# Kernel tuning notes

Measured on AMD Instinct MI355X. Metric: run time of the kernel, lower is better.

The kernel has to match this reference:

```python
import jax, jax.numpy as jnp
import numpy as np

N = 50000          # nodes
H = 202            # hidden = text(200) + selector(2)
E = 100000         # edges per forward edge type
FWD_TYPES = 3      # forward edge types; backward doubles to 6
LAYER_TIMESTEPS = (2,)
POS_MAX = 1024


def _pos_table():
    # transformer-style sinusoidal embeddings for positions [0, POS_MAX)
    inv_freq = 1.0 / (10000.0 ** (jnp.arange(0, H, 2, dtype=jnp.float32) / H))  # [H/2]
    pos = jnp.arange(POS_MAX, dtype=jnp.float32)
    sinusoid = pos[:, None] * inv_freq[None, :]                                  # [POS_MAX, H/2]
    return jnp.concatenate([jnp.sin(sinusoid), jnp.cos(sinusoid)], axis=-1)      # [POS_MAX, H]


def setup_inputs() -> dict:
    key = jax.random.key(0)
    ks = jax.random.split(key, 11)
    L = len(LAYER_TIMESTEPS)
    s = 0.1
    return {
        "node_states": jax.random.normal(ks[0], (N, H), jnp.float32),
        "edge_lists": jax.random.randint(ks[1], (FWD_TYPES, E, 2), 0, N, jnp.int32),
        "pos_lists": jax.random.randint(ks[2], (FWD_TYPES, E), 0, POS_MAX, jnp.int32),
        "msg_W": jax.random.normal(ks[3], (L, H, 2 * FWD_TYPES * H), jnp.float32) * s,
        "msg_b": jax.random.normal(ks[4], (L, 2 * FWD_TYPES * H), jnp.float32) * s,
        "pos_W": jax.random.normal(ks[5], (L, H, H), jnp.float32) * s,
        "pos_b": jax.random.normal(ks[6], (L, H), jnp.float32) * s,
        "gru_Wih": jax.random.normal(ks[7], (L, 3 * H, H), jnp.float32) * s,
        "gru_Whh": jax.random.normal(ks[8], (L, 3 * H, H), jnp.float32) * s,
        "gru_bih": jax.random.normal(ks[9], (L, 3 * H), jnp.float32) * s,
        "gru_bhh": jax.random.normal(ks[10], (L, 3 * H), jnp.float32) * s,
    }


def _ggnn(node_states, src, tgt, pos, divisor,
          msg_W, msg_b, pos_W, pos_b, gru_Wih, gru_Whh, gru_bih, gru_bhh):
    ET = src.shape[0]  # 2 * FWD_TYPES edge types (forward + backward)
    h = node_states
    pos_table = _pos_table()
    for l, steps in enumerate(LAYER_TIMESTEPS):
        # 2*sigmoid(pos_transform(position_embs)) gating, per position id
        gate = 2.0 * jax.nn.sigmoid(pos_table @ pos_W[l] + pos_b[l])  # [POS_MAX, H]
        for _ in range(steps):
            # fused per-edge-type transforms: [N, ET*H] chunked -> [N, ET, H]
            prop = (h @ msg_W[l] + msg_b[l]).reshape(h.shape[0], ET, H)
            messages = jnp.zeros_like(h)
            for i in range(ET):  # small fixed loop over edge types
                m = prop[:, i, :][src[i]] * gate[pos[i]]  # [E, H]
                messages = messages.at[tgt[i]].add(m)
            messages = messages / divisor  # mean aggregation
            # nn.GRUCell(messages, h)
            gi = messages @ gru_Wih[l].T + gru_bih[l]
            gh = h @ gru_Whh[l].T + gru_bhh[l]
            ir, iz, inn = jnp.split(gi, 3, axis=1)
            hr, hz, hn = jnp.split(gh, 3, axis=1)
            r = jax.nn.sigmoid(ir + hr)
            z = jax.nn.sigmoid(iz + hz)
            n = jnp.tanh(inn + r * hn)
            h = (1.0 - z) * n + z * h
    return h


def reference(node_states, edge_lists, pos_lists, msg_W, msg_b, pos_W, pos_b,
              gru_Wih, gru_Whh, gru_bih, gru_bhh):
    # backward edges = flipped forward edges; pos lists duplicated
    src = jnp.concatenate([edge_lists[:, :, 0], edge_lists[:, :, 1]], axis=0)  # [6, E]
    tgt = jnp.concatenate([edge_lists[:, :, 1], edge_lists[:, :, 0]], axis=0)  # [6, E]
    pos = jnp.clip(jnp.concatenate([pos_lists, pos_lists], axis=0), 0, POS_MAX - 1)
    # target bincount over all edge types; zero counts -> 1
    counts = jnp.zeros((node_states.shape[0],), jnp.float32).at[tgt.reshape(-1)].add(1.0)
    divisor = jnp.where(counts == 0, 1.0, counts)[:, None]
    out = _ggnn(node_states, src, tgt, pos, divisor, msg_W, msg_b, pos_W, pos_b,
                gru_Wih, gru_Whh, gru_bih, gru_bhh)
    return out, node_states
```

## Files before the change

### kernel.cpp

```cpp
#include <hip/hip_runtime.h>

#define NN 50000
#define HH 202
#define EE 100000
#define PMX 1024
#define NKT 7
#define PKS2 (16 * NKT * 64 * 8)
#define NEDG (6 * EE)
#define AFR (4 * NKT * 64 * 8)

typedef __attribute__((ext_vector_type(8))) short short8;
typedef __attribute__((ext_vector_type(4))) float v4f;

__device__ __forceinline__ float sigf(float x) { return 1.0f / (1.0f + expf(-x)); }

__device__ __forceinline__ unsigned short f2bf(float x) {
    unsigned int u = __float_as_uint(x);
    unsigned int r = (u + 0x7fffu + ((u >> 16) & 1u)) >> 16;
    return (unsigned short)r;
}
__device__ __forceinline__ float bf2f(unsigned short u) {
    return __uint_as_float(((unsigned int)u) << 16);
}

__device__ __forceinline__ int frag_off(int row, int k) {
    return (((row >> 4) * NKT + (k >> 5)) * 64 + ((k >> 3) & 3) * 16 + (row & 15)) * 8 + (k & 7);
}

__global__ void gate_kernel(const float* __restrict__ pos_W, const float* __restrict__ pos_b,
                            unsigned short* __restrict__ gate) {
    int p = blockIdx.x;
    __shared__ float pt[HH];
    int t = threadIdx.x;
    if (t < HH) {
        float v;
        if (t < 101) {
            float invf = expf(-(2.0f * t / 202.0f) * 9.210340371976184f);
            v = sinf((float)p * invf);
        } else {
            int k = t - 101;
            float invf = expf(-(2.0f * k / 202.0f) * 9.210340371976184f);
            v = cosf((float)p * invf);
        }
        pt[t] = v;
    }
    __syncthreads();
    for (int j = t; j < HH; j += blockDim.x) {
        float acc = pos_b[j];
        for (int k = 0; k < HH; ++k) acc += pt[k] * pos_W[k * HH + j];
        gate[p * HH + j] = f2bf(2.0f * sigf(acc));
    }
}

__global__ void pack_kernel(const float* __restrict__ S, int ldb, int row0, int col0, int mode,
                            unsigned short* __restrict__ BP) {
    int idx = blockIdx.x * blockDim.x + threadIdx.x;
    if (idx >= PKS2) return;
    int jj = idx & 7;
    int l = (idx >> 3) & 63;
    int r2 = idx >> 9;
    int cf = r2 / NKT, kt = r2 - cf * NKT;
    int k = kt * 32 + ((l >> 4) << 3) + jj;
    int j = cf * 16 + (l & 15);
    float v = 0.0f;
    if (k < HH && j < HH)
        v = mode ? S[(size_t)(row0 + j) * HH + k] : S[(size_t)k * ldb + col0 + j];
    BP[idx] = f2bf(v);
}

__global__ void count_kernel(const int* __restrict__ el, int* __restrict__ cnt) {
    int idx = blockIdx.x * blockDim.x + threadIdx.x;
    if (idx >= NEDG) return;
    int ty = idx / EE, e = idx - ty * EE;
    int2 pr = (ty < 3) ? reinterpret_cast<const int2*>(el)[ty * EE + e]
                       : reinterpret_cast<const int2*>(el)[(ty - 3) * EE + e];
    int tg = (ty < 3) ? pr.y : pr.x;
    atomicAdd(&cnt[tg], 1);
}

__global__ void scan1_kernel(const int* __restrict__ cnt, int* __restrict__ off,
                             int* __restrict__ bsum) {
    __shared__ int sd[256];
    int t = threadIdx.x, i = blockIdx.x * 256 + t;
    int v = (i < NN) ? cnt[i] : 0;
    sd[t] = v;
    __syncthreads();
    for (int s = 1; s < 256; s <<= 1) {
        int u = (t >= s) ? sd[t - s] : 0;
        __syncthreads();
        sd[t] += u;
        __syncthreads();
    }
    if (i < NN) off[i] = sd[t] - v;
    if (t == 255) bsum[blockIdx.x] = sd[255];
}

__global__ void scan2_kernel(int* __restrict__ bsum, int nb) {
    __shared__ int sd[256];
    int t = threadIdx.x;
    int v = (t < nb) ? bsum[t] : 0;
    sd[t] = v;
    __syncthreads();
    for (int s = 1; s < 256; s <<= 1) {
        int u = (t >= s) ? sd[t - s] : 0;
        __syncthreads();
        sd[t] += u;
        __syncthreads();
    }
    if (t < nb) bsum[t] = sd[t] - v;
}

__global__ void scan3_kernel(int* __restrict__ off, const int* __restrict__ bsum,
                             int* __restrict__ cursor) {
    int i = blockIdx.x * 256 + threadIdx.x;
    if (i < NN) {
        int o = off[i] + bsum[blockIdx.x];
        off[i] = o;
        cursor[i] = o;
    }
    if (i == 0) off[NN] = NEDG;
}

__global__ void inv_kernel(const int* __restrict__ cnt, float* __restrict__ inv) {
    int n = blockIdx.x * blockDim.x + threadIdx.x;
    if (n < NN) inv[n] = 1.0f / (float)max(cnt[n], 1);
}

__global__ void fill_kernel(const int* __restrict__ el, const int* __restrict__ pl,
                            int* __restrict__ cursor, int* __restrict__ edg) {
    int idx = blockIdx.x * blockDim.x + threadIdx.x;
    if (idx >= NEDG) return;
    int ty = idx / EE, e = idx - ty * EE;
    int s, tg;
    if (ty < 3) {
        int2 pr = reinterpret_cast<const int2*>(el)[ty * EE + e];
        s = pr.x; tg = pr.y;
    } else {
        int2 pr = reinterpret_cast<const int2*>(el)[(ty - 3) * EE + e];
        s = pr.y; tg = pr.x;
    }
    int p = pl[(ty % 3) * EE + e];
    p = min(max(p, 0), PMX - 1);
    int slot = atomicAdd(&cursor[tg], 1);
    edg[slot] = (s << 13) | (ty << 10) | p;
}

__global__ __launch_bounds__(512, 4) void gemm9(
    const void* __restrict__ Asrc, int a_is_f32,
    const unsigned short* __restrict__ BPbase, int npack,
    const float* __restrict__ bias,
    unsigned short* __restrict__ O0, unsigned short* __restrict__ O1, int split) {
    __shared__ alignas(16) unsigned short a_lds[AFR];
    __shared__ alignas(16) unsigned short c_lds[64 * HH];
    const int t = threadIdx.x;
    const int w = t >> 6;
    const int l = t & 63;
    const int lm = l & 15, lh = l >> 4;
    const int rowg = w >> 2, colg = w & 3;
    const int cs = colg * 4;
    const int base = blockIdx.x * 64;
    const int vrows = min(64, NN - base);
    const int nu4 = (vrows * 101) >> 2;

    if (a_is_f32) {
        const float* A = (const float*)Asrc;
        for (int idx = t; idx < 64 * 101; idx += 512) {
            int row = idx / 101;
            int c = idx - row * 101;
            int gn = base + row;
            float2 v = make_float2(0.f, 0.f);
            if (gn < NN) v = *reinterpret_cast<const float2*>(&A[(size_t)gn * HH + c * 2]);
            ushort2 bv; bv.x = f2bf(v.x); bv.y = f2bf(v.y);
            *reinterpret_cast<ushort2*>(&a_lds[frag_off(row, c * 2)]) = bv;
        }
    } else {
        const unsigned short* A = (const unsigned short*)Asrc;
        for (int idx = t; idx < 64 * 101; idx += 512) {
            int row = idx / 101;
            int c = idx - row * 101;
            int gn = base + row;
            ushort2 v; v.x = 0; v.y = 0;
            if (gn < NN) v = *reinterpret_cast<const ushort2*>(&A[(size_t)gn * HH + c * 2]);
            *reinterpret_cast<ushort2*>(&a_lds[frag_off(row, c * 2)]) = v;
        }
    }
    for (int idx = t; idx < 64 * 11; idx += 512) {
        int row = idx / 11;
        int c = idx - row * 11;
        ushort2 z; z.x = 0; z.y = 0;
        *reinterpret_cast<ushort2*>(&a_lds[frag_off(row, HH + c * 2)]) = z;
    }
    __syncthreads();

    const int aoff0 = (rowg * 2) * (NKT * 512) + l * 8;
    const int aoff1 = aoff0 + NKT * 512;

#pragma unroll 1
    for (int p = 0; p < npack; ++p) {
        const unsigned short* BP = BPbase + (size_t)p * PKS2 + (size_t)l * 8;
        v4f acc[4][2];
#pragma unroll
        for (int ci = 0; ci < 4; ++ci) {
            acc[ci][0] = (v4f){0.f, 0.f, 0.f, 0.f};
            acc[ci][1] = (v4f){0.f, 0.f, 0.f, 0.f};
        }

        short8 ac0 = *reinterpret_cast<const short8*>(&a_lds[aoff0]);
        short8 ac1 = *reinterpret_cast<const short8*>(&a_lds[aoff1]);
        short8 bc0 = *reinterpret_cast<const short8*>(BP + (size_t)(cs + 0) * NKT * 512);
        short8 bc1 = *reinterpret_cast<const short8*>(BP + (size_t)(cs + 1) * NKT * 512);
        short8 bc2 = *reinterpret_cast<const short8*>(BP + (size_t)(cs + 2) * NKT * 512);
        short8 bc3 = *reinterpret_cast<const short8*>(BP + (size_t)(cs + 3) * NKT * 512);

#pragma unroll
        for (int kt = 0; kt < NKT; ++kt) {
            const int kn = (kt + 1 < NKT) ? (kt + 1) : kt;
            const int ka = kn * 512;
            short8 an0 = *reinterpret_cast<const short8*>(&a_lds[aoff0 + ka]);
            short8 an1 = *reinterpret_cast<const short8*>(&a_lds[aoff1 + ka]);
            short8 bn0 = *reinterpret_cast<const short8*>(BP + (size_t)(cs + 0) * NKT * 512 + ka);
            short8 bn1 = *reinterpret_cast<const short8*>(BP + (size_t)(cs + 1) * NKT * 512 + ka);
            short8 bn2 = *reinterpret_cast<const short8*>(BP + (size_t)(cs + 2) * NKT * 512 + ka);
            short8 bn3 = *reinterpret_cast<const short8*>(BP + (size_t)(cs + 3) * NKT * 512 + ka);

            acc[0][0] = __builtin_amdgcn_mfma_f32_16x16x32_bf16(ac0, bc0, acc[0][0], 0, 0, 0);
            acc[0][1] = __builtin_amdgcn_mfma_f32_16x16x32_bf16(ac1, bc0, acc[0][1], 0, 0, 0);
            acc[1][0] = __builtin_amdgcn_mfma_f32_16x16x32_bf16(ac0, bc1, acc[1][0], 0, 0, 0);
            acc[1][1] = __builtin_amdgcn_mfma_f32_16x16x32_bf16(ac1, bc1, acc[1][1], 0, 0, 0);
            acc[2][0] = __builtin_amdgcn_mfma_f32_16x16x32_bf16(ac0, bc2, acc[2][0], 0, 0, 0);
            acc[2][1] = __builtin_amdgcn_mfma_f32_16x16x32_bf16(ac1, bc2, acc[2][1], 0, 0, 0);
            acc[3][0] = __builtin_amdgcn_mfma_f32_16x16x32_bf16(ac0, bc3, acc[3][0], 0, 0, 0);
            acc[3][1] = __builtin_amdgcn_mfma_f32_16x16x32_bf16(ac1, bc3, acc[3][1], 0, 0, 0);

            ac0 = an0; ac1 = an1;
            bc0 = bn0; bc1 = bn1; bc2 = bn2; bc3 = bn3;
        }

        __syncthreads();
#pragma unroll
        for (int ci = 0; ci < 4; ++ci) {
            int col = (cs + ci) * 16 + lm;
            if (col < HH) {
                float bb = bias ? bias[p * HH + col] : 0.0f;
#pragma unroll
                for (int rfi = 0; rfi < 2; ++rfi) {
#pragma unroll
                    for (int r = 0; r < 4; ++r)
                        c_lds[(rowg * 32 + rfi * 16 + lh * 4 + r) * HH + col] =
                            f2bf(acc[ci][rfi][r] + bb);
                }
            }
        }
        __syncthreads();

        unsigned short* slab = (p < split) ? O0 + (size_t)p * NN * HH
                                           : O1 + (size_t)(p - split) * NN * HH;
        uint4* dst = reinterpret_cast<uint4*>(slab + (size_t)base * HH);
        const uint4* srcp = reinterpret_cast<const uint4*>(c_lds);
        for (int i = t; i < nu4; i += 512) dst[i] = srcp[i];
    }
}

__global__ void agg_kernel(const unsigned short* __restrict__ CH0,
                           const unsigned short* __restrict__ CH45,
                           const int* __restrict__ off, const int* __restrict__ edg,
                           const unsigned short* __restrict__ gate,
                           const float* __restrict__ inv, unsigned short* __restrict__ msgb) {
    int n = blockIdx.x * 4 + (threadIdx.x >> 6);
    if (n >= NN) return;
    int lane = threadIdx.x & 63;
    int s0 = off[n], s1 = off[n + 1];
    int j0 = lane, j1 = lane + 64, j2 = lane + 128, j3 = lane + 192;
    bool j3ok = j3 < HH;
    float a0 = 0.f, a1 = 0.f, a2 = 0.f, a3 = 0.f;
    float b0 = 0.f, b1 = 0.f, b2 = 0.f, b3 = 0.f;
    int i = s0;
    for (; i + 1 < s1; i += 2) {
        int recA = edg[i], recB = edg[i + 1];
        int sA = recA >> 13, tyA = (recA >> 10) & 7, pA = recA & 1023;
        int sB = recB >> 13, tyB = (recB >> 10) & 7, pB = recB & 1023;
        const unsigned short* crA =
            ((tyA < 4) ? CH0 + (size_t)tyA * NN * HH : CH45 + (size_t)(tyA - 4) * NN * HH)
            + (size_t)sA * HH;
        const unsigned short* crB =
            ((tyB < 4) ? CH0 + (size_t)tyB * NN * HH : CH45 + (size_t)(tyB - 4) * NN * HH)
            + (size_t)sB * HH;
        const unsigned short* grA = gate + (size_t)pA * HH;
        const unsigned short* grB = gate + (size_t)pB * HH;
        a0 += bf2f(crA[j0]) * bf2f(grA[j0]);
        b0 += bf2f(crB[j0]) * bf2f(grB[j0]);
        a1 += bf2f(crA[j1]) * bf2f(grA[j1]);
        b1 += bf2f(crB[j1]) * bf2f(grB[j1]);
        a2 += bf2f(crA[j2]) * bf2f(grA[j2]);
        b2 += bf2f(crB[j2]) * bf2f(grB[j2]);
        if (j3ok) { a3 += bf2f(crA[j3]) * bf2f(grA[j3]);
                    b3 += bf2f(crB[j3]) * bf2f(grB[j3]); }
    }
    if (i < s1) {
        int rec = edg[i];
        int src = rec >> 13, ty = (rec >> 10) & 7, p = rec & 1023;
        const unsigned short* cr =
            ((ty < 4) ? CH0 + (size_t)ty * NN * HH : CH45 + (size_t)(ty - 4) * NN * HH)
            + (size_t)src * HH;
        const unsigned short* gr = gate + (size_t)p * HH;
        a0 += bf2f(cr[j0]) * bf2f(gr[j0]);
        a1 += bf2f(cr[j1]) * bf2f(gr[j1]);
        a2 += bf2f(cr[j2]) * bf2f(gr[j2]);
        if (j3ok) a3 += bf2f(cr[j3]) * bf2f(gr[j3]);
    }
    float iv = inv[n];
    unsigned short* mr = msgb + (size_t)n * HH;
    mr[j0] = f2bf((a0 + b0) * iv); mr[j1] = f2bf((a1 + b1) * iv);
    mr[j2] = f2bf((a2 + b2) * iv);
    if (j3ok) mr[j3] = f2bf((a3 + b3) * iv);
}

__global__ void gru_ew(float* __restrict__ h, const float* __restrict__ hsrc,
                       const unsigned short* __restrict__ GH,
                       const unsigned short* __restrict__ GIr,
                       const unsigned short* __restrict__ GIzn,
                       const float* __restrict__ bih, const float* __restrict__ bhh) {
    int n = blockIdx.x * 4 + (threadIdx.x >> 6);
    if (n >= NN) return;
    int lane = threadIdx.x & 63;
    const size_t NH = (size_t)NN * HH;
    const size_t ro = (size_t)n * HH;
    for (int j = lane; j < HH; j += 64) {
        float ghr = bf2f(GH[ro + j]);
        float ghz = bf2f(GH[NH + ro + j]);
        float ghn = bf2f(GH[2 * NH + ro + j]);
        float gir = bf2f(GIr[ro + j]);
        float giz = bf2f(GIzn[ro + j]);
        float gin = bf2f(GIzn[NH + ro + j]);
        float r = sigf(gir + ghr + bih[j] + bhh[j]);
        float z = sigf(giz + ghz + bih[202 + j] + bhh[202 + j]);
        float nn = tanhf(gin + bih[404 + j] + r * (ghn + bhh[404 + j]));
        h[ro + j] = (1.0f - z) * nn + z * hsrc[ro + j];
    }
}

extern "C" void kernel_launch(void* const* d_in, const int* in_sizes, int n_in,
                              void* d_out, int out_size, void* d_ws, size_t ws_size,
                              hipStream_t stream) {
    const float* node_states = (const float*)d_in[0];
    const int*   el          = (const int*)d_in[1];
    const int*   pl          = (const int*)d_in[2];
    const float* msg_W       = (const float*)d_in[3];
    const float* msg_b       = (const float*)d_in[4];
    const float* pos_W       = (const float*)d_in[5];
    const float* pos_b       = (const float*)d_in[6];
    const float* gWih        = (const float*)d_in[7];
    const float* gWhh        = (const float*)d_in[8];
    const float* gbih        = (const float*)d_in[9];
    const float* gbhh        = (const float*)d_in[10];

    float* out  = (float*)d_out;
    float* h    = out;
    float* out2 = out + (size_t)NN * HH;

    unsigned short* CH0  = (unsigned short*)d_ws;
    unsigned short* CH45 = (unsigned short*)out2;
    unsigned short* MSGB = CH0 + (size_t)4 * NN * HH;
    unsigned short* GATE = MSGB + (size_t)NN * HH;
    float* INV  = (float*)(GATE + (size_t)PMX * HH + 8);
    int* CNT    = (int*)(INV + NN);
    int* OFF    = CNT + NN;
    int* CUR    = OFF + NN + 4;
    int* BS     = CUR + NN;
    int* EDG    = BS + 256;
    unsigned short* BPA = (unsigned short*)(EDG + NEDG);
    unsigned short* BPp  = BPA;
    unsigned short* BPih = BPA + (size_t)6 * PKS2;
    unsigned short* BPhh = BPA + (size_t)9 * PKS2;

    const size_t NH = (size_t)NN * HH;
    hipMemsetAsync(CNT, 0, NN * sizeof(int), stream);
    gate_kernel<<<PMX, 256, 0, stream>>>(pos_W, pos_b, GATE);
    const int pkb = (PKS2 + 255) / 256;
    for (int ty = 0; ty < 6; ++ty)
        pack_kernel<<<pkb, 256, 0, stream>>>(msg_W, 1212, 0, ty * HH, 0, BPp + (size_t)ty * PKS2);
    pack_kernel<<<pkb, 256, 0, stream>>>(gWih, 0, 0,   0, 1, BPih);
    pack_kernel<<<pkb, 256, 0, stream>>>(gWih, 0, 202, 0, 1, BPih + PKS2);
    pack_kernel<<<pkb, 256, 0, stream>>>(gWih, 0, 404, 0, 1, BPih + 2 * PKS2);
    pack_kernel<<<pkb, 256, 0, stream>>>(gWhh, 0, 0,   0, 1, BPhh);
    pack_kernel<<<pkb, 256, 0, stream>>>(gWhh, 0, 202, 0, 1, BPhh + PKS2);
    pack_kernel<<<pkb, 256, 0, stream>>>(gWhh, 0, 404, 0, 1, BPhh + 2 * PKS2);

    const int nsb = (NN + 255) / 256;
    count_kernel<<<(NEDG + 255) / 256, 256, 0, stream>>>(el, CNT);
    scan1_kernel<<<nsb, 256, 0, stream>>>(CNT, OFF, BS);
    scan2_kernel<<<1, 256, 0, stream>>>(BS, nsb);
    scan3_kernel<<<nsb, 256, 0, stream>>>(OFF, BS, CUR);
    inv_kernel<<<nsb, 256, 0, stream>>>(CNT, INV);
    fill_kernel<<<(NEDG + 255) / 256, 256, 0, stream>>>(el, pl, CUR, EDG);

    const int gblocks = (NN + 63) / 64;
    const int ewblocks = (NN + 3) / 4;
    for (int step = 0; step < 2; ++step) {
        const float* hsrc = (step == 0) ? node_states : h;
        gemm9<<<gblocks, 512, 0, stream>>>(hsrc, 1, BPp, 6, msg_b, CH0, CH45, 4);
        agg_kernel<<<ewblocks, 256, 0, stream>>>(CH0, CH45, OFF, EDG, GATE, INV, MSGB);
        gemm9<<<gblocks, 512, 0, stream>>>(hsrc, 1, BPhh, 3, nullptr, CH0, nullptr, 4);
        gemm9<<<gblocks, 512, 0, stream>>>(MSGB, 0, BPih, 3, nullptr,
                                           CH0 + 3 * NH, CH45, 1);
        gru_ew<<<ewblocks, 256, 0, stream>>>(h, hsrc, CH0, CH0 + 3 * NH, CH45, gbih, gbhh);
    }
    hipMemcpyAsync(out2, node_states, NH * sizeof(float), hipMemcpyDeviceToDevice, stream);
}
```

Before: 660.1 us.

## Hold A tile in registers and compute 64x64 tiles per wave in GEMM

```diff
diff --git a/kernel.cpp b/kernel.cpp
--- a/kernel.cpp
+++ b/kernel.cpp
@@ -7,10 +7,11 @@
 #define NKT 7
 #define PKS2 (16 * NKT * 64 * 8)
 #define NEDG (6 * EE)
-#define AFR (4 * NKT * 64 * 8)
 
 typedef __attribute__((ext_vector_type(8))) short short8;
 typedef __attribute__((ext_vector_type(4))) float v4f;
+
+union U8 { unsigned int u[4]; short8 s; };
 
 __device__ __forceinline__ float sigf(float x) { return 1.0f / (1.0f + expf(-x)); }
 
@@ -23,8 +24,10 @@
     return __uint_as_float(((unsigned int)u) << 16);
 }
 
-__device__ __forceinline__ int frag_off(int row, int k) {
-    return (((row >> 4) * NKT + (k >> 5)) * 64 + ((k >> 3) & 3) * 16 + (row & 15)) * 8 + (k & 7);
+__device__ __forceinline__ unsigned int cvtpk(float lo, float hi) {
+    unsigned int r;
+    asm("v_cvt_pk_bf16_f32 %0, %1, %2" : "=v"(r) : "v"(lo), "v"(hi));
+    return r;
 }
 
 __global__ void gate_kernel(const float* __restrict__ pos_W, const float* __restrict__ pos_b,
@@ -145,68 +148,83 @@
     edg[slot] = (s << 13) | (ty << 10) | p;
 }
 
-__global__ __launch_bounds__(512, 4) void gemm9(
+__global__ __launch_bounds__(256, 2) void gemmR(
     const void* __restrict__ Asrc, int a_is_f32,
     const unsigned short* __restrict__ BPbase, int npack,
     const float* __restrict__ bias,
     unsigned short* __restrict__ O0, unsigned short* __restrict__ O1, int split) {
-    __shared__ alignas(16) unsigned short a_lds[AFR];
     __shared__ alignas(16) unsigned short c_lds[64 * HH];
     const int t = threadIdx.x;
     const int w = t >> 6;
     const int l = t & 63;
     const int lm = l & 15, lh = l >> 4;
-    const int rowg = w >> 2, colg = w & 3;
-    const int cs = colg * 4;
+    const int cs = w * 4;
     const int base = blockIdx.x * 64;
     const int vrows = min(64, NN - base);
     const int nu4 = (vrows * 101) >> 2;
 
+    short8 areg[4][7];
     if (a_is_f32) {
         const float* A = (const float*)Asrc;
-        for (int idx = t; idx < 64 * 101; idx += 512) {
-            int row = idx / 101;
-            int c = idx - row * 101;
-            int gn = base + row;
-            float2 v = make_float2(0.f, 0.f);
-            if (gn < NN) v = *reinterpret_cast<const float2*>(&A[(size_t)gn * HH + c * 2]);
-            ushort2 bv; bv.x = f2bf(v.x); bv.y = f2bf(v.y);
-            *reinterpret_cast<ushort2*>(&a_lds[frag_off(row, c * 2)]) = bv;
+#pragma unroll
+        for (int rf = 0; rf < 4; ++rf) {
+            int row = min(base + rf * 16 + lm, NN - 1);
+            const float* rp = A + (size_t)row * HH;
+#pragma unroll
+            for (int kt = 0; kt < NKT; ++kt) {
+                U8 u;
+                if (kt < 6) {
+                    const float2* p2 = (const float2*)(rp + kt * 32 + lh * 8);
+                    float2 v0 = p2[0], v1 = p2[1], v2 = p2[2], v3 = p2[3];
+                    u.u[0] = cvtpk(v0.x, v0.y); u.u[1] = cvtpk(v1.x, v1.y);
+                    u.u[2] = cvtpk(v2.x, v2.y); u.u[3] = cvtpk(v3.x, v3.y);
+                } else if (lh == 0) {
+                    const float2* p2 = (const float2*)(rp + 192);
+                    float2 v0 = p2[0], v1 = p2[1], v2 = p2[2], v3 = p2[3];
+                    u.u[0] = cvtpk(v0.x, v0.y); u.u[1] = cvtpk(v1.x, v1.y);
+                    u.u[2] = cvtpk(v2.x, v2.y); u.u[3] = cvtpk(v3.x, v3.y);
+                } else if (lh == 1) {
+                    float2 v = *(const float2*)(rp + 200);
+                    u.u[0] = cvtpk(v.x, v.y); u.u[1] = 0; u.u[2] = 0; u.u[3] = 0;
+                } else {
+                    u.u[0] = 0; u.u[1] = 0; u.u[2] = 0; u.u[3] = 0;
+                }
+                areg[rf][kt] = u.s;
+            }
         }
     } else {
         const unsigned short* A = (const unsigned short*)Asrc;
-        for (int idx = t; idx < 64 * 101; idx += 512) {
-            int row = idx / 101;
-            int c = idx - row * 101;
-            int gn = base + row;
-            ushort2 v; v.x = 0; v.y = 0;
-            if (gn < NN) v = *reinterpret_cast<const ushort2*>(&A[(size_t)gn * HH + c * 2]);
-            *reinterpret_cast<ushort2*>(&a_lds[frag_off(row, c * 2)]) = v;
+#pragma unroll
+        for (int rf = 0; rf < 4; ++rf) {
+            int row = min(base + rf * 16 + lm, NN - 1);
+            const unsigned int* rp = (const unsigned int*)(A + (size_t)row * HH);
+#pragma unroll
+            for (int kt = 0; kt < NKT; ++kt) {
+                U8 u;
+                int o = (kt * 32 + lh * 8) >> 1;
+                if (kt < 6) {
+                    u.u[0] = rp[o]; u.u[1] = rp[o + 1]; u.u[2] = rp[o + 2]; u.u[3] = rp[o + 3];
+                } else if (lh == 0) {
+                    u.u[0] = rp[96]; u.u[1] = rp[97]; u.u[2] = rp[98]; u.u[3] = rp[99];
+                } else if (lh == 1) {
+                    u.u[0] = rp[100]; u.u[1] = 0; u.u[2] = 0; u.u[3] = 0;
+                } else {
+                    u.u[0] = 0; u.u[1] = 0; u.u[2] = 0; u.u[3] = 0;
+                }
+                areg[rf][kt] = u.s;
+            }
         }
     }
-    for (int idx = t; idx < 64 * 11; idx += 512) {
-        int row = idx / 11;
-        int c = idx - row * 11;
-        ushort2 z; z.x = 0; z.y = 0;
-        *reinterpret_cast<ushort2*>(&a_lds[frag_off(row, HH + c * 2)]) = z;
-    }
-    __syncthreads();
-
-    const int aoff0 = (rowg * 2) * (NKT * 512) + l * 8;
-    const int aoff1 = aoff0 + NKT * 512;
 
 #pragma unroll 1
     for (int p = 0; p < npack; ++p) {
         const unsigned short* BP = BPbase + (size_t)p * PKS2 + (size_t)l * 8;
-        v4f acc[4][2];
-#pragma unroll
-        for (int ci = 0; ci < 4; ++ci) {
-            acc[ci][0] = (v4f){0.f, 0.f, 0.f, 0.f};
-            acc[ci][1] = (v4f){0.f, 0.f, 0.f, 0.f};
-        }
-
-        short8 ac0 = *reinterpret_cast<const short8*>(&a_lds[aoff0]);
-        short8 ac1 = *reinterpret_cast<const short8*>(&a_lds[aoff1]);
+        v4f acc[4][4];
+#pragma unroll
+        for (int ci = 0; ci < 4; ++ci)
+#pragma unroll
+            for (int rf = 0; rf < 4; ++rf) acc[ci][rf] = (v4f){0.f, 0.f, 0.f, 0.f};
+
         short8 bc0 = *reinterpret_cast<const short8*>(BP + (size_t)(cs + 0) * NKT * 512);
         short8 bc1 = *reinterpret_cast<const short8*>(BP + (size_t)(cs + 1) * NKT * 512);
         short8 bc2 = *reinterpret_cast<const short8*>(BP + (size_t)(cs + 2) * NKT * 512);
@@ -216,23 +234,28 @@
         for (int kt = 0; kt < NKT; ++kt) {
             const int kn = (kt + 1 < NKT) ? (kt + 1) : kt;
             const int ka = kn * 512;
-            short8 an0 = *reinterpret_cast<const short8*>(&a_lds[aoff0 + ka]);
-            short8 an1 = *reinterpret_cast<const short8*>(&a_lds[aoff1 + ka]);
             short8 bn0 = *reinterpret_cast<const short8*>(BP + (size_t)(cs + 0) * NKT * 512 + ka);
             short8 bn1 = *reinterpret_cast<const short8*>(BP + (size_t)(cs + 1) * NKT * 512 + ka);
             short8 bn2 = *reinterpret_cast<const short8*>(BP + (size_t)(cs + 2) * NKT * 512 + ka);
             short8 bn3 = *reinterpret_cast<const short8*>(BP + (size_t)(cs + 3) * NKT * 512 + ka);
 
-            acc[0][0] = __builtin_amdgcn_mfma_f32_16x16x32_bf16(ac0, bc0, acc[0][0], 0, 0, 0);
-            acc[0][1] = __builtin_amdgcn_mfma_f32_16x16x32_bf16(ac1, bc0, acc[0][1], 0, 0, 0);
-            acc[1][0] = __builtin_amdgcn_mfma_f32_16x16x32_bf16(ac0, bc1, acc[1][0], 0, 0, 0);
-            acc[1][1] = __builtin_amdgcn_mfma_f32_16x16x32_bf16(ac1, bc1, acc[1][1], 0, 0, 0);
-            acc[2][0] = __builtin_amdgcn_mfma_f32_16x16x32_bf16(ac0, bc2, acc[2][0], 0, 0, 0);
-            acc[2][1] = __builtin_amdgcn_mfma_f32_16x16x32_bf16(ac1, bc2, acc[2][1], 0, 0, 0);
-            acc[3][0] = __builtin_amdgcn_mfma_f32_16x16x32_bf16(ac0, bc3, acc[3][0], 0, 0, 0);
-            acc[3][1] = __builtin_amdgcn_mfma_f32_16x16x32_bf16(ac1, bc3, acc[3][1], 0, 0, 0);
-
-            ac0 = an0; ac1 = an1;
+            acc[0][0] = __builtin_amdgcn_mfma_f32_16x16x32_bf16(areg[0][kt], bc0, acc[0][0], 0, 0, 0);
+            acc[0][1] = __builtin_amdgcn_mfma_f32_16x16x32_bf16(areg[1][kt], bc0, acc[0][1], 0, 0, 0);
+            acc[0][2] = __builtin_amdgcn_mfma_f32_16x16x32_bf16(areg[2][kt], bc0, acc[0][2], 0, 0, 0);
+            acc[0][3] = __builtin_amdgcn_mfma_f32_16x16x32_bf16(areg[3][kt], bc0, acc[0][3], 0, 0, 0);
+            acc[1][0] = __builtin_amdgcn_mfma_f32_16x16x32_bf16(areg[0][kt], bc1, acc[1][0], 0, 0, 0);
+            acc[1][1] = __builtin_amdgcn_mfma_f32_16x16x32_bf16(areg[1][kt], bc1, acc[1][1], 0, 0, 0);
+            acc[1][2] = __builtin_amdgcn_mfma_f32_16x16x32_bf16(areg[2][kt], bc1, acc[1][2], 0, 0, 0);
+            acc[1][3] = __builtin_amdgcn_mfma_f32_16x16x32_bf16(areg[3][kt], bc1, acc[1][3], 0, 0, 0);
+            acc[2][0] = __builtin_amdgcn_mfma_f32_16x16x32_bf16(areg[0][kt], bc2, acc[2][0], 0, 0, 0);
+            acc[2][1] = __builtin_amdgcn_mfma_f32_16x16x32_bf16(areg[1][kt], bc2, acc[2][1], 0, 0, 0);
+            acc[2][2] = __builtin_amdgcn_mfma_f32_16x16x32_bf16(areg[2][kt], bc2, acc[2][2], 0, 0, 0);
+            acc[2][3] = __builtin_amdgcn_mfma_f32_16x16x32_bf16(areg[3][kt], bc2, acc[2][3], 0, 0, 0);
+            acc[3][0] = __builtin_amdgcn_mfma_f32_16x16x32_bf16(areg[0][kt], bc3, acc[3][0], 0, 0, 0);
+            acc[3][1] = __builtin_amdgcn_mfma_f32_16x16x32_bf16(areg[1][kt], bc3, acc[3][1], 0, 0, 0);
+            acc[3][2] = __builtin_amdgcn_mfma_f32_16x16x32_bf16(areg[2][kt], bc3, acc[3][2], 0, 0, 0);
+            acc[3][3] = __builtin_amdgcn_mfma_f32_16x16x32_bf16(areg[3][kt], bc3, acc[3][3], 0, 0, 0);
+
             bc0 = bn0; bc1 = bn1; bc2 = bn2; bc3 = bn3;
         }
 
@@ -243,11 +266,10 @@
             if (col < HH) {
                 float bb = bias ? bias[p * HH + col] : 0.0f;
 #pragma unroll
-                for (int rfi = 0; rfi < 2; ++rfi) {
+                for (int rf = 0; rf < 4; ++rf) {
 #pragma unroll
                     for (int r = 0; r < 4; ++r)
-                        c_lds[(rowg * 32 + rfi * 16 + lh * 4 + r) * HH + col] =
-                            f2bf(acc[ci][rfi][r] + bb);
+                        c_lds[(rf * 16 + lh * 4 + r) * HH + col] = f2bf(acc[ci][rf][r] + bb);
                 }
             }
         }
@@ -257,7 +279,7 @@
                                            : O1 + (size_t)(p - split) * NN * HH;
         uint4* dst = reinterpret_cast<uint4*>(slab + (size_t)base * HH);
         const uint4* srcp = reinterpret_cast<const uint4*>(c_lds);
-        for (int i = t; i < nu4; i += 512) dst[i] = srcp[i];
+        for (int i = t; i < nu4; i += 256) dst[i] = srcp[i];
     }
 }
 
@@ -398,10 +420,10 @@
     const int ewblocks = (NN + 3) / 4;
     for (int step = 0; step < 2; ++step) {
         const float* hsrc = (step == 0) ? node_states : h;
-        gemm9<<<gblocks, 512, 0, stream>>>(hsrc, 1, BPp, 6, msg_b, CH0, CH45, 4);
+        gemmR<<<gblocks, 256, 0, stream>>>(hsrc, 1, BPp, 6, msg_b, CH0, CH45, 4);
         agg_kernel<<<ewblocks, 256, 0, stream>>>(CH0, CH45, OFF, EDG, GATE, INV, MSGB);
-        gemm9<<<gblocks, 512, 0, stream>>>(hsrc, 1, BPhh, 3, nullptr, CH0, nullptr, 4);
-        gemm9<<<gblocks, 512, 0, stream>>>(MSGB, 0, BPih, 3, nullptr,
+        gemmR<<<gblocks, 256, 0, stream>>>(hsrc, 1, BPhh, 3, nullptr, CH0, nullptr, 4);
+        gemmR<<<gblocks, 256, 0, stream>>>(MSGB, 0, BPih, 3, nullptr,
                                            CH0 + 3 * NH, CH45, 1);
         gru_ew<<<ewblocks, 256, 0, stream>>>(h, hsrc, CH0, CH0 + 3 * NH, CH45, gbih, gbhh);
     }
```

Result: slower. 699.3 us (+5.9%).
